# Optimization experiments

Measured on AMD Instinct MI355X. Metric: run time of the kernel, lower is better.

Reference implementation:

```python
import jax, jax.numpy as jnp
import numpy as np


def _hungarian(cost):
    """Min-cost assignment for square cost [n, n] (Jonker-Volgenant style, O(n^3)).
    Returns col[r] = column assigned to row r (matches scipy linear_sum_assignment
    col_ind for square matrices; row_ind is implicitly arange(n))."""
    n = cost.shape[0]
    u = np.zeros(n + 1)
    v = np.zeros(n + 1)
    p = np.zeros(n + 1, dtype=np.int64)   # p[j] = row matched to column j (1-based)
    way = np.zeros(n + 1, dtype=np.int64)
    for i in range(1, n + 1):
        p[0] = i
        j0 = 0
        minv = np.full(n + 1, np.inf)
        used = np.zeros(n + 1, dtype=bool)
        while True:
            used[j0] = True
            i0 = p[j0]
            cur = cost[i0 - 1] - u[i0] - v[1:]
            free = ~used[1:]
            better = free & (cur < minv[1:])
            minv[1:][better] = cur[better]
            way[1:][better] = j0
            masked = np.where(free, minv[1:], np.inf)
            j1 = int(np.argmin(masked)) + 1
            delta = masked[j1 - 1]
            u[p[used]] += delta
            v[used] -= delta
            minv[1:][free] -= delta
            j0 = j1
            if p[j0] == 0:
                break
        while j0:
            j1 = way[j0]
            p[j0] = p[j1]
            j0 = j1
    col = np.empty(n, dtype=np.int64)
    for j in range(1, n + 1):
        col[p[j] - 1] = j - 1
    return col


def _pairwise_cost(seq1, seq2):
    # cost[b, j, i] = ||seq1[b, i] - seq2[b, j]||_2  (matches torch.stack(cost, 1))
    sq1 = jnp.sum(seq1 * seq1, axis=-1)                 # [B, N]
    sq2 = jnp.sum(seq2 * seq2, axis=-1)                 # [B, N]
    inner = jnp.einsum('bjd,bid->bji', seq2, seq1)      # [B, N, N]
    d2 = sq2[:, :, None] + sq1[:, None, :] - 2.0 * inner
    return jnp.sqrt(jnp.maximum(d2, 0.0))


def setup_inputs() -> dict:
    key = jax.random.key(0)
    k1, k2 = jax.random.split(key)
    B, N, D = 64, 256, 512
    seq1 = jax.random.normal(k1, (B, N, D), dtype=jnp.float32)
    seq2 = jax.random.normal(k2, (B, N, D), dtype=jnp.float32)
    return {"seq1": seq1, "seq2": seq2}


def reference(seq1, seq2):
    B, N, D = seq1.shape
    cost = _pairwise_cost(seq1, seq2)                   # [B, N, N], rows=j (seq2), cols=i (seq1)
    cost_np = np.asarray(cost)
    # Hungarian solve is inherently host-side (original calls scipy on .numpy()).
    col_idx = jnp.asarray(np.stack([_hungarian(cost_np[b]) for b in range(B)]))  # [B, N]
    # Square cost -> row_ind = arange, so reorder_1 = seq1 transposed to [B, D, N].
    reorder_1 = jnp.swapaxes(seq1, 1, 2)
    gathered = jnp.take_along_axis(seq2, col_idx[:, :, None], axis=1)  # [B, N, D]
    reorder_2 = jnp.swapaxes(gathered, 1, 2)            # [B, D, N]
    return (reorder_1, reorder_2)
```

## Files before the change

kernel.cpp:

```cpp
#include <hip/hip_runtime.h>
#include <cstddef>
#include <cmath>

#define BATCH 64
#define NPTS  256
#define DIM   512

__global__ __launch_bounds__(256) void norms_kernel(const float* __restrict__ x,
                                                    float* __restrict__ out) {
  const int w = threadIdx.x >> 6, lane = threadIdx.x & 63;
  const int r = blockIdx.x * 4 + w;
  const float4* row = reinterpret_cast<const float4*>(x + (size_t)r * DIM);
  float4 v0 = row[lane];
  float4 v1 = row[lane + 64];
  float s = v0.x*v0.x + v0.y*v0.y + v0.z*v0.z + v0.w*v0.w
          + v1.x*v1.x + v1.y*v1.y + v1.z*v1.z + v1.w*v1.w;
#pragma unroll
  for (int off = 32; off; off >>= 1) s += __shfl_xor(s, off);
  if (lane == 0) out[r] = s;
}

#define BM 64
#define BN 64
#define BK 32
__global__ __launch_bounds__(256) void cost_kernel(const float* __restrict__ seq1,
                                                   const float* __restrict__ seq2,
                                                   const float* __restrict__ sq1,
                                                   const float* __restrict__ sq2,
                                                   float* __restrict__ cost) {
  const int b  = blockIdx.z;
  const int j0 = blockIdx.y * BM;
  const int i0 = blockIdx.x * BN;
  const int t  = threadIdx.x;
  const int tx = t & 15, ty = t >> 4;

  __shared__ float As[BK][BM + 1];
  __shared__ float Bs[BK][BN + 1];

  const float* A  = seq2 + ((size_t)b * NPTS + j0) * DIM;
  const float* Bp = seq1 + ((size_t)b * NPTS + i0) * DIM;

  float acc[4][4] = {};

  for (int k0 = 0; k0 < DIM; k0 += BK) {
#pragma unroll
    for (int l = 0; l < 2; ++l) {
      int f  = t + l * 256;
      int r  = f >> 3;
      int c4 = (f & 7) * 4;
      float4 a  = *reinterpret_cast<const float4*>(A  + (size_t)r * DIM + k0 + c4);
      float4 bb = *reinterpret_cast<const float4*>(Bp + (size_t)r * DIM + k0 + c4);
      As[c4 + 0][r] = a.x;  As[c4 + 1][r] = a.y;  As[c4 + 2][r] = a.z;  As[c4 + 3][r] = a.w;
      Bs[c4 + 0][r] = bb.x; Bs[c4 + 1][r] = bb.y; Bs[c4 + 2][r] = bb.z; Bs[c4 + 3][r] = bb.w;
    }
    __syncthreads();
#pragma unroll
    for (int kk = 0; kk < BK; ++kk) {
      float a[4], bb[4];
#pragma unroll
      for (int q = 0; q < 4; ++q) a[q]  = As[kk][ty * 4 + q];
#pragma unroll
      for (int q = 0; q < 4; ++q) bb[q] = Bs[kk][tx * 4 + q];
#pragma unroll
      for (int x = 0; x < 4; ++x)
#pragma unroll
        for (int y = 0; y < 4; ++y) acc[x][y] += a[x] * bb[y];
    }
    __syncthreads();
  }

#pragma unroll
  for (int x = 0; x < 4; ++x) {
    int j = j0 + ty * 4 + x;
    float s2 = sq2[b * NPTS + j];
    float4 o;
    float r0 = s2 + sq1[b * NPTS + i0 + tx * 4 + 0] - 2.f * acc[x][0];
    float r1 = s2 + sq1[b * NPTS + i0 + tx * 4 + 1] - 2.f * acc[x][1];
    float r2 = s2 + sq1[b * NPTS + i0 + tx * 4 + 2] - 2.f * acc[x][2];
    float r3 = s2 + sq1[b * NPTS + i0 + tx * 4 + 3] - 2.f * acc[x][3];
    o.x = sqrtf(fmaxf(r0, 0.f)); o.y = sqrtf(fmaxf(r1, 0.f));
    o.z = sqrtf(fmaxf(r2, 0.f)); o.w = sqrtf(fmaxf(r3, 0.f));
    *reinterpret_cast<float4*>(cost + ((size_t)b * NPTS + j) * NPTS + i0 + tx * 4) = o;
  }
}

__global__ __launch_bounds__(64) void hungarian_kernel(const float* __restrict__ cost,
                                                       int* __restrict__ col_out) {
  const int b    = blockIdx.x;
  const int lane = threadIdx.x;
  const int c0   = lane * 4;
  const float* C = cost + (size_t)b * NPTS * NPTS;

  __shared__ double u_sh[NPTS + 1];
  __shared__ int    p_sh[NPTS + 1];
  __shared__ int    way_sh[NPTS + 1];
  __shared__ int    rowclaim[NPTS];
  __shared__ int    freerows[NPTS];
  __shared__ int    nfree_sh;

  for (int t = lane; t <= NPTS; t += 64) { u_sh[t] = 0.0; p_sh[t] = 0; way_sh[t] = 0; }
  for (int t = lane; t < NPTS; t += 64) rowclaim[t] = -1;
  if (lane == 0) nfree_sh = 0;
  __syncthreads();

  float vm0 = INFINITY, vm1 = INFINITY, vm2 = INFINITY, vm3 = INFINITY;
  int   bi0 = 0, bi1 = 0, bi2 = 0, bi3 = 0;
#pragma unroll 4
  for (int i = 0; i < NPTS; ++i) {
    float4 cr = *reinterpret_cast<const float4*>(C + (size_t)i * NPTS + c0);
    if (cr.x < vm0) { vm0 = cr.x; bi0 = i; }
    if (cr.y < vm1) { vm1 = cr.y; bi1 = i; }
    if (cr.z < vm2) { vm2 = cr.z; bi2 = i; }
    if (cr.w < vm3) { vm3 = cr.w; bi3 = i; }
  }
  double v[4] = { (double)vm0, (double)vm1, (double)vm2, (double)vm3 };

  int got0 = atomicCAS(&rowclaim[bi0], -1, c0 + 0);
  int got1 = atomicCAS(&rowclaim[bi1], -1, c0 + 1);
  int got2 = atomicCAS(&rowclaim[bi2], -1, c0 + 2);
  int got3 = atomicCAS(&rowclaim[bi3], -1, c0 + 3);
  p_sh[c0 + 1] = (got0 == -1) ? bi0 + 1 : 0;
  p_sh[c0 + 2] = (got1 == -1) ? bi1 + 1 : 0;
  p_sh[c0 + 3] = (got2 == -1) ? bi2 + 1 : 0;
  p_sh[c0 + 4] = (got3 == -1) ? bi3 + 1 : 0;
  __syncthreads();

#pragma unroll
  for (int k = 0; k < 4; ++k) {
    int r = c0 + k;
    if (rowclaim[r] == -1) { int s = atomicAdd(&nfree_sh, 1); freerows[s] = r + 1; }
  }
  __syncthreads();
  const int nfree = nfree_sh;

  int pr0 = p_sh[c0 + 1], pr1 = p_sh[c0 + 2], pr2 = p_sh[c0 + 3], pr3 = p_sh[c0 + 4];

  for (int fi = 0; fi < nfree; ++fi) {
    const int i = freerows[fi];
    if (lane == 0) p_sh[0] = i;
    double minv[4] = { HUGE_VAL, HUGE_VAL, HUGE_VAL, HUGE_VAL };
    unsigned usedmask = 0;
    int j0 = 0, i0 = i;

    for (int it = 0; it <= NPTS; ++it) {
      if (j0 > 0) {
        int c = j0 - 1;
        if ((c >> 2) == lane) usedmask |= 1u << (c & 3);
      }
      double ui = u_sh[i0];
      float4 cr = *reinterpret_cast<const float4*>(C + (size_t)(i0 - 1) * NPTS + c0);
      float cf[4] = { cr.x, cr.y, cr.z, cr.w };

      double val = HUGE_VAL; int idx = 0;
#pragma unroll
      for (int k = 0; k < 4; ++k) {
        if (!((usedmask >> k) & 1u)) {
          double cur = (double)cf[k] - ui - v[k];
          if (cur < minv[k]) { minv[k] = cur; way_sh[c0 + k + 1] = j0; }
          if (minv[k] < val) { val = minv[k]; idx = c0 + k + 1; }
        }
      }
#pragma unroll
      for (int off = 32; off; off >>= 1) {
        double oval = __shfl_xor(val, off);
        int    oidx = __shfl_xor(idx, off);
        if (oval < val || (oval == val && oidx < idx)) { val = oval; idx = oidx; }
      }
      const double delta = val; const int j1 = idx;
      if (j1 == 0) { j0 = 0; break; }

#pragma unroll
      for (int k = 0; k < 4; ++k) {
        if ((usedmask >> k) & 1u) {
          int pm = (k == 0) ? pr0 : (k == 1) ? pr1 : (k == 2) ? pr2 : pr3;
          u_sh[pm] += delta;
          v[k] -= delta;
        } else {
          minv[k] -= delta;
        }
      }
      if (lane == 0) u_sh[i] += delta;

      j0 = j1;
      int ksel = (j1 - 1) & 3, src = (j1 - 1) >> 2;
      int cand = pr0;
      cand = (ksel == 1) ? pr1 : cand;
      cand = (ksel == 2) ? pr2 : cand;
      cand = (ksel == 3) ? pr3 : cand;
      int pj = __shfl(cand, src);
      if (pj == 0) break;
      i0 = pj;
    }

    __syncthreads();
    if (lane == 0) {
      int jj = j0;
      for (int guard = 0; jj && guard <= NPTS; ++guard) {
        int jn = way_sh[jj];
        p_sh[jj] = p_sh[jn];
        jj = jn;
      }
    }
    __syncthreads();
    pr0 = p_sh[c0 + 1]; pr1 = p_sh[c0 + 2]; pr2 = p_sh[c0 + 3]; pr3 = p_sh[c0 + 4];
  }

  __syncthreads();
  for (int j = lane + 1; j <= NPTS; j += 64) {
    int pj  = p_sh[j];
    int dst = (pj >= 1 && pj <= NPTS) ? pj - 1 : j - 1;
    col_out[b * NPTS + dst] = j - 1;
  }
}

__global__ __launch_bounds__(256) void transpose_kernel(const float* __restrict__ in,
                                                        float* __restrict__ out) {
  __shared__ float tile[32][33];
  const int b  = blockIdx.z;
  const int d0 = blockIdx.x * 32, n0 = blockIdx.y * 32;
  const int tx = threadIdx.x & 31, ty = threadIdx.x >> 5;
  const float* ip = in  + (size_t)b * NPTS * DIM;
  float*       op = out + (size_t)b * DIM * NPTS;
#pragma unroll
  for (int q = 0; q < 4; ++q)
    tile[ty + q * 8][tx] = ip[(size_t)(n0 + ty + q * 8) * DIM + d0 + tx];
  __syncthreads();
#pragma unroll
  for (int q = 0; q < 4; ++q)
    op[(size_t)(d0 + ty + q * 8) * NPTS + n0 + tx] = tile[tx][ty + q * 8];
}

__global__ __launch_bounds__(256) void gather_transpose_kernel(const float* __restrict__ in,
                                                               const int* __restrict__ idx,
                                                               float* __restrict__ out) {
  __shared__ float tile[32][33];
  __shared__ int   rows[32];
  const int b  = blockIdx.z;
  const int d0 = blockIdx.x * 32, n0 = blockIdx.y * 32;
  const int tx = threadIdx.x & 31, ty = threadIdx.x >> 5;
  if (threadIdx.x < 32) {
    int r = idx[b * NPTS + n0 + threadIdx.x];
    rows[threadIdx.x] = ((unsigned)r < NPTS) ? r : 0;
  }
  __syncthreads();
  const float* ip = in  + (size_t)b * NPTS * DIM;
  float*       op = out + (size_t)b * DIM * NPTS;
#pragma unroll
  for (int q = 0; q < 4; ++q)
    tile[ty + q * 8][tx] = ip[(size_t)rows[ty + q * 8] * DIM + d0 + tx];
  __syncthreads();
#pragma unroll
  for (int q = 0; q < 4; ++q)
    op[(size_t)(d0 + ty + q * 8) * NPTS + n0 + tx] = tile[tx][ty + q * 8];
}

extern "C" void kernel_launch(void* const* d_in, const int* in_sizes, int n_in,
                              void* d_out, int out_size, void* d_ws, size_t ws_size,
                              hipStream_t stream) {
  const float* seq1 = (const float*)d_in[0];
  const float* seq2 = (const float*)d_in[1];
  float* out1 = (float*)d_out;
  float* out2 = out1 + (size_t)BATCH * DIM * NPTS;

  char*  ws     = (char*)d_ws;
  float* cost   = (float*)ws;
  float* sq1    = (float*)(ws + (size_t)BATCH * NPTS * NPTS * 4);
  float* sq2    = sq1 + BATCH * NPTS;
  int*   colidx = (int*)(sq2 + BATCH * NPTS);

  norms_kernel<<<BATCH * NPTS / 4, 256, 0, stream>>>(seq1, sq1);
  norms_kernel<<<BATCH * NPTS / 4, 256, 0, stream>>>(seq2, sq2);
  cost_kernel<<<dim3(NPTS / BN, NPTS / BM, BATCH), 256, 0, stream>>>(seq1, seq2, sq1, sq2, cost);
  hungarian_kernel<<<BATCH, 64, 0, stream>>>(cost, colidx);
  transpose_kernel<<<dim3(DIM / 32, NPTS / 32, BATCH), 256, 0, stream>>>(seq1, out1);
  gather_transpose_kernel<<<dim3(DIM / 32, NPTS / 32, BATCH), 256, 0, stream>>>(seq2, colidx, out2);
}
```

Measured before the change: 6.572 ms.

## Keep Hungarian duals and matching in registers, derive row potential via shuffle

Removes the shared-memory u, p and way arrays from the Hungarian kernel. The row potential u[i0] is recomputed from the tight edge as cost minus v of the column just reached, and is broadcast with a wave shuffle. Matching and back-pointer state now live in per-lane registers, and path augmentation walks the chain with shuffles instead of a serial lane-0 loop between barriers. This cuts LDS traffic and synchronisation in the serial inner loop. The cost is extra shuffles, and u is rebuilt from float cost minus double v, which may differ slightly numerically.

```diff
diff --git a/kernel.cpp b/kernel.cpp
--- a/kernel.cpp
+++ b/kernel.cpp
@@ -91,40 +91,35 @@
   const int c0   = lane * 4;
   const float* C = cost + (size_t)b * NPTS * NPTS;
 
-  __shared__ double u_sh[NPTS + 1];
-  __shared__ int    p_sh[NPTS + 1];
-  __shared__ int    way_sh[NPTS + 1];
-  __shared__ int    rowclaim[NPTS];
-  __shared__ int    freerows[NPTS];
-  __shared__ int    nfree_sh;
-
-  for (int t = lane; t <= NPTS; t += 64) { u_sh[t] = 0.0; p_sh[t] = 0; way_sh[t] = 0; }
+  __shared__ int rowclaim[NPTS];
+  __shared__ int freerows[NPTS];
+  __shared__ int nfree_sh;
+
   for (int t = lane; t < NPTS; t += 64) rowclaim[t] = -1;
   if (lane == 0) nfree_sh = 0;
   __syncthreads();
 
-  float vm0 = INFINITY, vm1 = INFINITY, vm2 = INFINITY, vm3 = INFINITY;
-  int   bi0 = 0, bi1 = 0, bi2 = 0, bi3 = 0;
+  float vm[4] = {INFINITY, INFINITY, INFINITY, INFINITY};
+  int   bi[4] = {0, 0, 0, 0};
 #pragma unroll 4
   for (int i = 0; i < NPTS; ++i) {
     float4 cr = *reinterpret_cast<const float4*>(C + (size_t)i * NPTS + c0);
-    if (cr.x < vm0) { vm0 = cr.x; bi0 = i; }
-    if (cr.y < vm1) { vm1 = cr.y; bi1 = i; }
-    if (cr.z < vm2) { vm2 = cr.z; bi2 = i; }
-    if (cr.w < vm3) { vm3 = cr.w; bi3 = i; }
-  }
-  double v[4] = { (double)vm0, (double)vm1, (double)vm2, (double)vm3 };
-
-  int got0 = atomicCAS(&rowclaim[bi0], -1, c0 + 0);
-  int got1 = atomicCAS(&rowclaim[bi1], -1, c0 + 1);
-  int got2 = atomicCAS(&rowclaim[bi2], -1, c0 + 2);
-  int got3 = atomicCAS(&rowclaim[bi3], -1, c0 + 3);
-  p_sh[c0 + 1] = (got0 == -1) ? bi0 + 1 : 0;
-  p_sh[c0 + 2] = (got1 == -1) ? bi1 + 1 : 0;
-  p_sh[c0 + 3] = (got2 == -1) ? bi2 + 1 : 0;
-  p_sh[c0 + 4] = (got3 == -1) ? bi3 + 1 : 0;
-  __syncthreads();
-
+    float cf[4] = {cr.x, cr.y, cr.z, cr.w};
+#pragma unroll
+    for (int k = 0; k < 4; ++k)
+      if (cf[k] < vm[k]) { vm[k] = cf[k]; bi[k] = i; }
+  }
+  double v[4];
+  int    pr[4];
+#pragma unroll
+  for (int k = 0; k < 4; ++k) v[k] = (double)vm[k];
+
+#pragma unroll
+  for (int k = 0; k < 4; ++k) {
+    int got = atomicCAS(&rowclaim[bi[k]], -1, c0 + k);
+    pr[k] = (got == -1) ? bi[k] + 1 : 0;
+  }
+  __syncthreads();
 #pragma unroll
   for (int k = 0; k < 4; ++k) {
     int r = c0 + k;
@@ -133,30 +128,32 @@
   __syncthreads();
   const int nfree = nfree_sh;
 
-  int pr0 = p_sh[c0 + 1], pr1 = p_sh[c0 + 2], pr2 = p_sh[c0 + 3], pr3 = p_sh[c0 + 4];
-
   for (int fi = 0; fi < nfree; ++fi) {
     const int i = freerows[fi];
-    if (lane == 0) p_sh[0] = i;
-    double minv[4] = { HUGE_VAL, HUGE_VAL, HUGE_VAL, HUGE_VAL };
+    double minv[4] = {HUGE_VAL, HUGE_VAL, HUGE_VAL, HUGE_VAL};
+    int    way[4]  = {0, 0, 0, 0};
     unsigned usedmask = 0;
     int j0 = 0, i0 = i;
 
     for (int it = 0; it <= NPTS; ++it) {
+      const int ksel = (j0 - 1) & 3, src = (j0 - 1) >> 2;
+      if (j0 > 0 && src == lane) usedmask |= 1u << ksel;
+
+      float4 cr = *reinterpret_cast<const float4*>(C + (size_t)(i0 - 1) * NPTS + c0);
+      float cf[4] = {cr.x, cr.y, cr.z, cr.w};
+
+      double u_i0 = 0.0;
       if (j0 > 0) {
-        int c = j0 - 1;
-        if ((c >> 2) == lane) usedmask |= 1u << (c & 3);
-      }
-      double ui = u_sh[i0];
-      float4 cr = *reinterpret_cast<const float4*>(C + (size_t)(i0 - 1) * NPTS + c0);
-      float cf[4] = { cr.x, cr.y, cr.z, cr.w };
+        double cand = (double)cf[ksel] - v[ksel];
+        u_i0 = __shfl(cand, src);
+      }
 
       double val = HUGE_VAL; int idx = 0;
 #pragma unroll
       for (int k = 0; k < 4; ++k) {
         if (!((usedmask >> k) & 1u)) {
-          double cur = (double)cf[k] - ui - v[k];
-          if (cur < minv[k]) { minv[k] = cur; way_sh[c0 + k + 1] = j0; }
+          double cur = (double)cf[k] - u_i0 - v[k];
+          if (cur < minv[k]) { minv[k] = cur; way[k] = j0; }
           if (minv[k] < val) { val = minv[k]; idx = c0 + k + 1; }
         }
       }
@@ -171,45 +168,49 @@
 
 #pragma unroll
       for (int k = 0; k < 4; ++k) {
-        if ((usedmask >> k) & 1u) {
-          int pm = (k == 0) ? pr0 : (k == 1) ? pr1 : (k == 2) ? pr2 : pr3;
-          u_sh[pm] += delta;
-          v[k] -= delta;
-        } else {
-          minv[k] -= delta;
-        }
-      }
-      if (lane == 0) u_sh[i] += delta;
+        if ((usedmask >> k) & 1u) v[k] -= delta; else minv[k] -= delta;
+      }
 
       j0 = j1;
-      int ksel = (j1 - 1) & 3, src = (j1 - 1) >> 2;
-      int cand = pr0;
-      cand = (ksel == 1) ? pr1 : cand;
-      cand = (ksel == 2) ? pr2 : cand;
-      cand = (ksel == 3) ? pr3 : cand;
-      int pj = __shfl(cand, src);
+      int ks = (j1 - 1) & 3, sr = (j1 - 1) >> 2;
+      int cand = pr[0];
+      cand = (ks == 1) ? pr[1] : cand;
+      cand = (ks == 2) ? pr[2] : cand;
+      cand = (ks == 3) ? pr[3] : cand;
+      int pj = __shfl(cand, sr);
       if (pj == 0) break;
       i0 = pj;
     }
 
-    __syncthreads();
-    if (lane == 0) {
-      int jj = j0;
-      for (int guard = 0; jj && guard <= NPTS; ++guard) {
-        int jn = way_sh[jj];
-        p_sh[jj] = p_sh[jn];
-        jj = jn;
-      }
-    }
-    __syncthreads();
-    pr0 = p_sh[c0 + 1]; pr1 = p_sh[c0 + 2]; pr2 = p_sh[c0 + 3]; pr3 = p_sh[c0 + 4];
-  }
-
-  __syncthreads();
-  for (int j = lane + 1; j <= NPTS; j += 64) {
-    int pj  = p_sh[j];
-    int dst = (pj >= 1 && pj <= NPTS) ? pj - 1 : j - 1;
-    col_out[b * NPTS + dst] = j - 1;
+    int jj = j0;
+    for (int guard = 0; jj && guard <= NPTS; ++guard) {
+      int ks = (jj - 1) & 3, sr = (jj - 1) >> 2;
+      int wc = way[0];
+      wc = (ks == 1) ? way[1] : wc;
+      wc = (ks == 2) ? way[2] : wc;
+      wc = (ks == 3) ? way[3] : wc;
+      int jn = __shfl(wc, sr);
+      int pv;
+      if (jn == 0) {
+        pv = i;
+      } else {
+        int ks2 = (jn - 1) & 3, sr2 = (jn - 1) >> 2;
+        int pc = pr[0];
+        pc = (ks2 == 1) ? pr[1] : pc;
+        pc = (ks2 == 2) ? pr[2] : pc;
+        pc = (ks2 == 3) ? pr[3] : pc;
+        pv = __shfl(pc, sr2);
+      }
+      if (sr == lane) pr[ks] = pv;
+      jj = jn;
+    }
+  }
+
+#pragma unroll
+  for (int k = 0; k < 4; ++k) {
+    int pj  = pr[k];
+    int dst = (pj >= 1 && pj <= NPTS) ? pj - 1 : c0 + k;
+    col_out[b * NPTS + dst] = c0 + k;
   }
 }
 
```

Result: faster. 5.483 ms (-16.6%).
